# Optimization experiments

Measured on AMD Instinct MI355X. Metric: run time of the kernel, lower is better.

The kernel has to match this reference:

```python
import jax, jax.numpy as jnp
import numpy as np

N = 8  # node_count, complete graph
# edge list exactly as in __init__: all (i, j) with i != j, row-major order
_edges = np.array([[i, j] for i in range(N) for j in range(N) if i != j], dtype=np.int32)
SRC = jnp.asarray(_edges[:, 0])  # edge_index[0]
DST = jnp.asarray(_edges[:, 1])  # edge_index[1]


def gcn_norm_adj(edge_w):
    """Dense normalized adjacency D^-1/2 (A + I) D^-1/2 with edge weights, as in PyG GCNConv."""
    A = jnp.zeros((N, N), edge_w.dtype).at[DST, SRC].set(edge_w) + jnp.eye(N, dtype=edge_w.dtype)
    deg = A.sum(axis=1)  # in-degree (weights into each target node, incl. self loop)
    dinv = jnp.where(deg > 0, deg ** -0.5, 0.0)
    return dinv[:, None] * A * dinv[None, :]


def setup_inputs() -> dict:
    key = jax.random.key(0)
    ks = jax.random.split(key, 4)
    B, F_, H, O = 8192, 512, 256, 128
    return {
        "latent_vec": jax.random.normal(ks[0], (B, F_), jnp.float32),
        "node_features": jax.random.normal(ks[1], (N, F_), jnp.float32) * 0.1,
        "edge_attr": jnp.ones((N * (N - 1), 1), jnp.float32),
        "W1": jax.random.normal(ks[2], (F_, H), jnp.float32) / np.sqrt(F_),
        "b1": jnp.zeros((H,), jnp.float32),
        "W2": jax.random.normal(ks[3], (H, O), jnp.float32) / np.sqrt(H),
        "b2": jnp.zeros((O,), jnp.float32),
    }


def reference(latent_vec, node_features, edge_attr, W1, b1, W2, b2):
    # update_graph_with_latent: per-sample softmax perturbation of shared node features
    w = jax.nn.softmax(latent_vec[:, :N], axis=1)[..., None]        # [B, N, 1]
    X = node_features[None, :, :] + 0.1 * w                          # [B, N, F]
    A_hat = gcn_norm_adj(edge_attr[:, 0])                            # [N, N], shared across batch
    # GCNConv1 + ReLU (dropout is identity in eval mode)
    h = jax.nn.relu(jnp.einsum('ij,bjh->bih', A_hat, X @ W1) + b1)   # [B, N, H]
    # GCNConv2
    o = jnp.einsum('ij,bjo->bio', A_hat, h @ W2) + b2                # [B, N, O]
    return o.mean(axis=1)                                            # [B, O]
```

## Files before the change

kernel.cpp:

```cpp
#include <hip/hip_runtime.h>

#define NNODE 8
#define FDIM 512
#define HDIM 256
#define ODIM 128
#define BATCH 8192
#define SPB 16
#define NBLK (BATCH / SPB)

#define OCH 16
#define QCH (ODIM / OCH)
#define NGR 64
#define CHK (HDIM / NGR)

#define OFF_TAU  0
#define OFF_AHAT (NNODE * HDIM)
#define OFF_TAB  (OFF_AHAT + 128)

__global__ __launch_bounds__(1024) void gnn_build(
    const float* __restrict__ nf, const float* __restrict__ W1,
    const float* __restrict__ ea, const float* __restrict__ b1,
    const float* __restrict__ W2, const float* __restrict__ b2,
    float* __restrict__ ws)
{
    const int tid = threadIdx.x;
    const int j = blockIdx.x >> 3;
    const int q = blockIdx.x & (QCH - 1);
    const int obase = q * OCH;

    __shared__ float v_s[FDIM];
    __shared__ float pp_s[4][HDIM];
    __shared__ float ss_s[4][HDIM];
    __shared__ float A_s[64], dinv_s[NNODE], m_s[NNODE];
    __shared__ float P_s[HDIM], k_s[HDIM], tau_s[HDIM];
    __shared__ int   hs_s[HDIM];
    __shared__ int   rp_s[4][HDIM];
    __shared__ float pe_s[HDIM], ke_s[HDIM], bp_s[HDIM], bk_s[HDIM];
    __shared__ float cta[NGR][OCH], ctb[NGR][OCH], eta[NGR][OCH], etb[NGR][OCH];

    if (tid < 64) {
        int i = tid >> 3, qn = tid & 7;
        float a = (i == qn) ? 1.f : 0.f;
        if (i != qn) a += ea[qn * 7 + i - (i > qn ? 1 : 0)];
        A_s[tid] = a;
    }
    __syncthreads();
    if (tid < NNODE) {
        float d = 0.f;
#pragma unroll
        for (int qq = 0; qq < NNODE; qq++) d += A_s[tid * 8 + qq];
        dinv_s[tid] = d > 0.f ? 1.0f / sqrtf(d) : 0.f;
    }
    __syncthreads();
    if (tid < 64) {
        int i = tid >> 3, qn = tid & 7;
        A_s[tid] = dinv_s[i] * A_s[tid] * dinv_s[qn];
    }
    __syncthreads();
    if (tid < NNODE) {
        float mm = 0.f;
#pragma unroll
        for (int i = 0; i < NNODE; i++) mm += A_s[i * 8 + tid];
        m_s[tid] = mm * 0.125f;
    }
    if (tid < FDIM) {
        float v = 0.f;
#pragma unroll
        for (int n = 0; n < NNODE; n++) v = fmaf(A_s[j * 8 + n], nf[n * FDIM + tid], v);
        v_s[tid] = v;
    }
    __syncthreads();

    {
        const int h = tid & 255;
        const int g = tid >> 8;
        const float* Wp = W1 + (g * 128) * HDIM + h;
        const float* vp = v_s + g * 128;
        float pp = 0.f, ss = 0.f;
#pragma unroll 16
        for (int ff = 0; ff < 128; ff++) {
            float w = Wp[ff * HDIM];
            pp = fmaf(vp[ff], w, pp);
            ss += w;
        }
        pp_s[g][h] = pp;
        ss_s[g][h] = ss;
    }
    __syncthreads();

    if (tid < HDIM) {
        float P = b1[tid] + ((pp_s[0][tid] + pp_s[1][tid]) + (pp_s[2][tid] + pp_s[3][tid]));
        float s1 = ((ss_s[0][tid] + ss_s[1][tid]) + (ss_s[2][tid] + ss_s[3][tid]));
        float kap = 0.1f * s1;
        float tau = (kap != 0.f) ? (-P / kap) : __builtin_inff();
        P_s[tid] = P;
        k_s[tid] = kap;
        tau_s[tid] = tau;
        float mj = m_s[j];
        bp_s[tid] = mj * ((kap < 0.f || (kap == 0.f && P > 0.f)) ? P : 0.f);
        bk_s[tid] = mj * ((kap < 0.f) ? kap : 0.f);
    }
    __syncthreads();

    {
        const int h = tid & 255, kq = tid >> 8;
        float th = tau_s[h];
        int r = 0;
        for (int k = kq * 64; k < kq * 64 + 64; k++) {
            float tk = tau_s[k];
            r += (tk < th) || (tk == th && k < h);
        }
        rp_s[kq][h] = r;
    }
    __syncthreads();
    if (tid < HDIM) {
        int r = rp_s[0][tid] + rp_s[1][tid] + rp_s[2][tid] + rp_s[3][tid];
        hs_s[r] = tid;
        if (q == 0) ws[OFF_TAU + j * HDIM + r] = tau_s[tid];
    }
    if (blockIdx.x == 0 && tid >= 256 && tid < 320)
        ws[OFF_AHAT + tid - 256] = A_s[tid - 256];
    __syncthreads();
    if (tid < HDIM) {
        int h2 = hs_s[tid];
        float kk = k_s[h2], pp = P_s[h2];
        float sgn = (kk > 0.f) ? 1.f : ((kk < 0.f) ? -1.f : 0.f);
        float mj = m_s[j];
        pe_s[tid] = mj * sgn * pp;
        ke_s[tid] = mj * sgn * kk;
    }
    __syncthreads();

    const int oc = tid & (OCH - 1);
    const int rr = tid >> 4;
    {
        float ba = 0.f, bb = 0.f, sa = 0.f, sb = 0.f;
#pragma unroll
        for (int k = 0; k < CHK; k++) {
            int h = rr * CHK + k;
            float wb = W2[h * ODIM + obase + oc];
            ba = fmaf(bp_s[h], wb, ba);
            bb = fmaf(bk_s[h], wb, bb);
            float we = W2[hs_s[h] * ODIM + obase + oc];
            sa = fmaf(pe_s[h], we, sa);
            sb = fmaf(ke_s[h], we, sb);
        }
        cta[rr][oc] = ba; ctb[rr][oc] = bb;
        eta[rr][oc] = sa; etb[rr][oc] = sb;
    }
    __syncthreads();

    float2* TAB = (float2*)(ws + OFF_TAB);

    if (tid < OCH) {
        const int o = tid;
        float accA = 0.f, accB = 0.f;
#pragma unroll
        for (int g = 0; g < NGR; g++) { accA += cta[g][o]; accB += ctb[g][o]; }
        if (j == 0) accA += b2[obase + o];
        TAB[(size_t)(j * 257) * ODIM + obase + o] = make_float2(accA, accB);
#pragma unroll
        for (int g = 0; g < NGR; g++) {
            float ta = eta[g][o], tb = etb[g][o];
            eta[g][o] = accA; etb[g][o] = accB;
            accA += ta; accB += tb;
        }
    }
    __syncthreads();

    {
        float ra = eta[rr][oc], rb = etb[rr][oc];
#pragma unroll
        for (int k = 0; k < CHK; k++) {
            int r = rr * CHK + k;
            float we = W2[hs_s[r] * ODIM + obase + oc];
            ra = fmaf(pe_s[r], we, ra);
            rb = fmaf(ke_s[r], we, rb);
            TAB[(size_t)(j * 257 + r + 1) * ODIM + obase + oc] = make_float2(ra, rb);
        }
    }
}

__global__ __launch_bounds__(256) void gnn_main(const float* __restrict__ latent,
                                                const float* __restrict__ ws,
                                                float* __restrict__ out) {
    const int t = threadIdx.x;
    const int bs = blockIdx.x * SPB;

    __shared__ float tau_s[NNODE][HDIM];
    __shared__ float A_s[64];
    __shared__ float lat_s[SPB][NNODE];
    __shared__ float cc_s[SPB][NNODE];
    __shared__ int   rr_s[SPB][NNODE];

    for (int k = t; k < NNODE * HDIM; k += 256)
        ((float*)tau_s)[k] = ws[OFF_TAU + k];
    if (t < 64) A_s[t] = ws[OFF_AHAT + t];
    if (t >= 128) {
        int u = t - 128;
        int s = u >> 3, qq = u & 7;
        lat_s[s][qq] = latent[(size_t)(bs + s) * FDIM + qq];
    }
    __syncthreads();

    if (t < SPB * NNODE) {
        int s = t >> 3, i = t & 7;
        float mx = -1e30f;
#pragma unroll
        for (int qq = 0; qq < NNODE; qq++) mx = fmaxf(mx, lat_s[s][qq]);
        float sum = 0.f, acc = 0.f;
#pragma unroll
        for (int qq = 0; qq < NNODE; qq++) {
            float e = expf(lat_s[s][qq] - mx);
            sum += e;
            acc = fmaf(A_s[i * NNODE + qq], e, acc);
        }
        float c = acc / sum;
        cc_s[s][i] = c;
        int lo = 0, hi = HDIM;
        while (lo < hi) {
            int mid = (lo + hi) >> 1;
            if (tau_s[i][mid] < c) lo = mid + 1; else hi = mid;
        }
        rr_s[s][i] = lo;
    }
    __syncthreads();

    const int o = t & (ODIM - 1);
    const int sh = t >> 7;
    const float2* TAB = (const float2*)(ws + OFF_TAB);

#pragma unroll 2
    for (int s = sh; s < SPB; s += 2) {
        float acc = 0.f;
#pragma unroll
        for (int jj = 0; jj < NNODE; jj++) {
            int r = rr_s[s][jj];
            float c = cc_s[s][jj];
            float2 ab = TAB[(size_t)(jj * 257 + r) * ODIM + o];
            acc += fmaf(c, ab.y, ab.x);
        }
        out[(size_t)(bs + s) * ODIM + o] = acc;
    }
}

extern "C" void kernel_launch(void* const* d_in, const int* in_sizes, int n_in,
                              void* d_out, int out_size, void* d_ws, size_t ws_size,
                              hipStream_t stream) {
    const float* latent = (const float*)d_in[0];
    const float* nf     = (const float*)d_in[1];
    const float* ea     = (const float*)d_in[2];
    const float* W1     = (const float*)d_in[3];
    const float* b1     = (const float*)d_in[4];
    const float* W2     = (const float*)d_in[5];
    const float* b2     = (const float*)d_in[6];
    float* out = (float*)d_out;
    float* ws  = (float*)d_ws;

    hipLaunchKernelGGL(gnn_build, dim3(NNODE * QCH), dim3(1024), 0, stream,
                       nf, W1, ea, b1, W2, b2, ws);
    hipLaunchKernelGGL(gnn_main, dim3(NBLK), dim3(256), 0, stream, latent, ws, out);
}
```

Before: 25.73 us.

## Fuse build and main kernels into one launch with an atomic flag barrier

Merges the table-building kernel and the per-sample lookup kernel into a single 256-thread launch. The first 64 blocks build the tables and bump a global counter, and every block spins on that counter before reading the tables. Softmax and latent loading overlap with the build phase. The build work moves from 1024-thread to 256-thread blocks, so each thread does more serial work in the W1 reduction and the rank sort. It also adds a memset and relies on all build blocks being resident alongside the spinning ones, which risks a deadlock or long stalls.

```diff
diff --git a/kernel.cpp b/kernel.cpp
--- a/kernel.cpp
+++ b/kernel.cpp
@@ -10,33 +10,42 @@
 
 #define OCH 16
 #define QCH (ODIM / OCH)
-#define NGR 64
+#define NGR 16
 #define CHK (HDIM / NGR)
+#define NBUILD (NNODE * QCH)
 
 #define OFF_TAU  0
-#define OFF_AHAT (NNODE * HDIM)
-#define OFF_TAB  (OFF_AHAT + 128)
-
-__global__ __launch_bounds__(1024) void gnn_build(
-    const float* __restrict__ nf, const float* __restrict__ W1,
+#define OFF_TAB  (NNODE * HDIM)
+#define OFF_FLAG (OFF_TAB + NNODE * 257 * ODIM * 2)
+
+__global__ __launch_bounds__(256, 2) void gnn_one(
+    const float* __restrict__ latent, const float* __restrict__ nf,
     const float* __restrict__ ea, const float* __restrict__ b1,
-    const float* __restrict__ W2, const float* __restrict__ b2,
-    float* __restrict__ ws)
+    const float* __restrict__ W1, const float* __restrict__ W2,
+    const float* __restrict__ b2, float* __restrict__ ws,
+    float* __restrict__ out)
 {
     const int tid = threadIdx.x;
-    const int j = blockIdx.x >> 3;
-    const int q = blockIdx.x & (QCH - 1);
-    const int obase = q * OCH;
-
+    const int b = blockIdx.x;
+    const int bs = b * SPB;
+
+    __shared__ float A_s[64], dinv_s[NNODE], m_s[NNODE];
+    __shared__ float lat_s[SPB][NNODE];
+    __shared__ float cc_s[SPB][NNODE];
+    __shared__ int   rr_s[SPB][NNODE];
+    __shared__ float tau_m[NNODE][HDIM];
     __shared__ float v_s[FDIM];
-    __shared__ float pp_s[4][HDIM];
-    __shared__ float ss_s[4][HDIM];
-    __shared__ float A_s[64], dinv_s[NNODE], m_s[NNODE];
-    __shared__ float P_s[HDIM], k_s[HDIM], tau_s[HDIM];
+    __shared__ float P_s[HDIM], k_s[HDIM], tau_b[HDIM];
     __shared__ int   hs_s[HDIM];
-    __shared__ int   rp_s[4][HDIM];
     __shared__ float pe_s[HDIM], ke_s[HDIM], bp_s[HDIM], bk_s[HDIM];
     __shared__ float cta[NGR][OCH], ctb[NGR][OCH], eta[NGR][OCH], etb[NGR][OCH];
+
+    unsigned int* flag = (unsigned int*)(ws + OFF_FLAG);
+
+    if (tid >= 128) {
+        int u = tid - 128;
+        lat_s[u >> 3][u & 7] = latent[(size_t)(bs + (u >> 3)) * FDIM + (u & 7)];
+    }
 
     if (tid < 64) {
         int i = tid >> 3, qn = tid & 7;
@@ -63,148 +72,10 @@
         for (int i = 0; i < NNODE; i++) mm += A_s[i * 8 + tid];
         m_s[tid] = mm * 0.125f;
     }
-    if (tid < FDIM) {
-        float v = 0.f;
-#pragma unroll
-        for (int n = 0; n < NNODE; n++) v = fmaf(A_s[j * 8 + n], nf[n * FDIM + tid], v);
-        v_s[tid] = v;
-    }
-    __syncthreads();
-
-    {
-        const int h = tid & 255;
-        const int g = tid >> 8;
-        const float* Wp = W1 + (g * 128) * HDIM + h;
-        const float* vp = v_s + g * 128;
-        float pp = 0.f, ss = 0.f;
-#pragma unroll 16
-        for (int ff = 0; ff < 128; ff++) {
-            float w = Wp[ff * HDIM];
-            pp = fmaf(vp[ff], w, pp);
-            ss += w;
-        }
-        pp_s[g][h] = pp;
-        ss_s[g][h] = ss;
-    }
-    __syncthreads();
-
-    if (tid < HDIM) {
-        float P = b1[tid] + ((pp_s[0][tid] + pp_s[1][tid]) + (pp_s[2][tid] + pp_s[3][tid]));
-        float s1 = ((ss_s[0][tid] + ss_s[1][tid]) + (ss_s[2][tid] + ss_s[3][tid]));
-        float kap = 0.1f * s1;
-        float tau = (kap != 0.f) ? (-P / kap) : __builtin_inff();
-        P_s[tid] = P;
-        k_s[tid] = kap;
-        tau_s[tid] = tau;
-        float mj = m_s[j];
-        bp_s[tid] = mj * ((kap < 0.f || (kap == 0.f && P > 0.f)) ? P : 0.f);
-        bk_s[tid] = mj * ((kap < 0.f) ? kap : 0.f);
-    }
-    __syncthreads();
-
-    {
-        const int h = tid & 255, kq = tid >> 8;
-        float th = tau_s[h];
-        int r = 0;
-        for (int k = kq * 64; k < kq * 64 + 64; k++) {
-            float tk = tau_s[k];
-            r += (tk < th) || (tk == th && k < h);
-        }
-        rp_s[kq][h] = r;
-    }
-    __syncthreads();
-    if (tid < HDIM) {
-        int r = rp_s[0][tid] + rp_s[1][tid] + rp_s[2][tid] + rp_s[3][tid];
-        hs_s[r] = tid;
-        if (q == 0) ws[OFF_TAU + j * HDIM + r] = tau_s[tid];
-    }
-    if (blockIdx.x == 0 && tid >= 256 && tid < 320)
-        ws[OFF_AHAT + tid - 256] = A_s[tid - 256];
-    __syncthreads();
-    if (tid < HDIM) {
-        int h2 = hs_s[tid];
-        float kk = k_s[h2], pp = P_s[h2];
-        float sgn = (kk > 0.f) ? 1.f : ((kk < 0.f) ? -1.f : 0.f);
-        float mj = m_s[j];
-        pe_s[tid] = mj * sgn * pp;
-        ke_s[tid] = mj * sgn * kk;
-    }
-    __syncthreads();
-
-    const int oc = tid & (OCH - 1);
-    const int rr = tid >> 4;
-    {
-        float ba = 0.f, bb = 0.f, sa = 0.f, sb = 0.f;
-#pragma unroll
-        for (int k = 0; k < CHK; k++) {
-            int h = rr * CHK + k;
-            float wb = W2[h * ODIM + obase + oc];
-            ba = fmaf(bp_s[h], wb, ba);
-            bb = fmaf(bk_s[h], wb, bb);
-            float we = W2[hs_s[h] * ODIM + obase + oc];
-            sa = fmaf(pe_s[h], we, sa);
-            sb = fmaf(ke_s[h], we, sb);
-        }
-        cta[rr][oc] = ba; ctb[rr][oc] = bb;
-        eta[rr][oc] = sa; etb[rr][oc] = sb;
-    }
-    __syncthreads();
-
-    float2* TAB = (float2*)(ws + OFF_TAB);
-
-    if (tid < OCH) {
-        const int o = tid;
-        float accA = 0.f, accB = 0.f;
-#pragma unroll
-        for (int g = 0; g < NGR; g++) { accA += cta[g][o]; accB += ctb[g][o]; }
-        if (j == 0) accA += b2[obase + o];
-        TAB[(size_t)(j * 257) * ODIM + obase + o] = make_float2(accA, accB);
-#pragma unroll
-        for (int g = 0; g < NGR; g++) {
-            float ta = eta[g][o], tb = etb[g][o];
-            eta[g][o] = accA; etb[g][o] = accB;
-            accA += ta; accB += tb;
-        }
-    }
-    __syncthreads();
-
-    {
-        float ra = eta[rr][oc], rb = etb[rr][oc];
-#pragma unroll
-        for (int k = 0; k < CHK; k++) {
-            int r = rr * CHK + k;
-            float we = W2[hs_s[r] * ODIM + obase + oc];
-            ra = fmaf(pe_s[r], we, ra);
-            rb = fmaf(ke_s[r], we, rb);
-            TAB[(size_t)(j * 257 + r + 1) * ODIM + obase + oc] = make_float2(ra, rb);
-        }
-    }
-}
-
-__global__ __launch_bounds__(256) void gnn_main(const float* __restrict__ latent,
-                                                const float* __restrict__ ws,
-                                                float* __restrict__ out) {
-    const int t = threadIdx.x;
-    const int bs = blockIdx.x * SPB;
-
-    __shared__ float tau_s[NNODE][HDIM];
-    __shared__ float A_s[64];
-    __shared__ float lat_s[SPB][NNODE];
-    __shared__ float cc_s[SPB][NNODE];
-    __shared__ int   rr_s[SPB][NNODE];
-
-    for (int k = t; k < NNODE * HDIM; k += 256)
-        ((float*)tau_s)[k] = ws[OFF_TAU + k];
-    if (t < 64) A_s[t] = ws[OFF_AHAT + t];
-    if (t >= 128) {
-        int u = t - 128;
-        int s = u >> 3, qq = u & 7;
-        lat_s[s][qq] = latent[(size_t)(bs + s) * FDIM + qq];
-    }
-    __syncthreads();
-
-    if (t < SPB * NNODE) {
-        int s = t >> 3, i = t & 7;
+
+    float c_keep = 0.f;
+    if (tid < SPB * NNODE) {
+        int s = tid >> 3, i = tid & 7;
         float mx = -1e30f;
 #pragma unroll
         for (int qq = 0; qq < NNODE; qq++) mx = fmaxf(mx, lat_s[s][qq]);
@@ -215,19 +86,151 @@
             sum += e;
             acc = fmaf(A_s[i * NNODE + qq], e, acc);
         }
-        float c = acc / sum;
-        cc_s[s][i] = c;
+        c_keep = acc / sum;
+        cc_s[s][i] = c_keep;
+    }
+
+    if (b < NBUILD) {
+        const int j = b >> 3;
+        const int q = b & (QCH - 1);
+        const int obase = q * OCH;
+
+        {
+            float aj[NNODE];
+#pragma unroll
+            for (int n = 0; n < NNODE; n++) aj[n] = A_s[j * 8 + n];
+#pragma unroll
+            for (int u = 0; u < 2; u++) {
+                int f = tid + u * 256;
+                float v = 0.f;
+#pragma unroll
+                for (int n = 0; n < NNODE; n++) v = fmaf(aj[n], nf[n * FDIM + f], v);
+                v_s[f] = v;
+            }
+        }
+        __syncthreads();
+
+        {
+            const float* Wc = W1 + tid;
+            float pp = 0.f, ss = 0.f;
+#pragma unroll 8
+            for (int f = 0; f < FDIM; f++) {
+                float w = Wc[(size_t)f * HDIM];
+                pp = fmaf(v_s[f], w, pp);
+                ss += w;
+            }
+            float P = b1[tid] + pp;
+            float kap = 0.1f * ss;
+            float tau = (kap != 0.f) ? (-P / kap) : __builtin_inff();
+            P_s[tid] = P;
+            k_s[tid] = kap;
+            tau_b[tid] = tau;
+            float mj = m_s[j];
+            bp_s[tid] = mj * ((kap < 0.f || (kap == 0.f && P > 0.f)) ? P : 0.f);
+            bk_s[tid] = mj * ((kap < 0.f) ? kap : 0.f);
+        }
+        __syncthreads();
+
+        {
+            float th = tau_b[tid];
+            int r = 0;
+            for (int k = 0; k < HDIM; k++) {
+                float tk = tau_b[k];
+                r += (tk < th) || (tk == th && k < tid);
+            }
+            hs_s[r] = tid;
+            if (q == 0) ws[OFF_TAU + j * HDIM + r] = th;
+        }
+        __syncthreads();
+        {
+            int h2 = hs_s[tid];
+            float kk = k_s[h2], pp = P_s[h2];
+            float sgn = (kk > 0.f) ? 1.f : ((kk < 0.f) ? -1.f : 0.f);
+            float mj = m_s[j];
+            pe_s[tid] = mj * sgn * pp;
+            ke_s[tid] = mj * sgn * kk;
+        }
+        __syncthreads();
+
+        const int oc = tid & (OCH - 1);
+        const int rr = tid >> 4;
+        {
+            float ba = 0.f, bb = 0.f, sa = 0.f, sb = 0.f;
+#pragma unroll
+            for (int k = 0; k < CHK; k++) {
+                int h = rr * CHK + k;
+                float wb = W2[h * ODIM + obase + oc];
+                ba = fmaf(bp_s[h], wb, ba);
+                bb = fmaf(bk_s[h], wb, bb);
+                float we = W2[hs_s[h] * ODIM + obase + oc];
+                sa = fmaf(pe_s[h], we, sa);
+                sb = fmaf(ke_s[h], we, sb);
+            }
+            cta[rr][oc] = ba; ctb[rr][oc] = bb;
+            eta[rr][oc] = sa; etb[rr][oc] = sb;
+        }
+        __syncthreads();
+
+        float2* TAB = (float2*)(ws + OFF_TAB);
+
+        if (tid < OCH) {
+            const int o = tid;
+            float accA = 0.f, accB = 0.f;
+#pragma unroll
+            for (int g = 0; g < NGR; g++) { accA += cta[g][o]; accB += ctb[g][o]; }
+            if (j == 0) accA += b2[obase + o];
+            TAB[(size_t)(j * 257) * ODIM + obase + o] = make_float2(accA, accB);
+#pragma unroll
+            for (int g = 0; g < NGR; g++) {
+                float ta = eta[g][o], tb = etb[g][o];
+                eta[g][o] = accA; etb[g][o] = accB;
+                accA += ta; accB += tb;
+            }
+        }
+        __syncthreads();
+
+        {
+            float ra = eta[rr][oc], rb = etb[rr][oc];
+#pragma unroll
+            for (int k = 0; k < CHK; k++) {
+                int r = rr * CHK + k;
+                float we = W2[hs_s[r] * ODIM + obase + oc];
+                ra = fmaf(pe_s[r], we, ra);
+                rb = fmaf(ke_s[r], we, rb);
+                TAB[(size_t)(j * 257 + r + 1) * ODIM + obase + oc] = make_float2(ra, rb);
+            }
+        }
+        __syncthreads();
+        if (tid == 0)
+            __hip_atomic_fetch_add(flag, 1u, __ATOMIC_RELEASE, __HIP_MEMORY_SCOPE_AGENT);
+    }
+
+    if (tid == 0) {
+        while (__hip_atomic_fetch_add(flag, 0u, __ATOMIC_RELAXED,
+                                      __HIP_MEMORY_SCOPE_AGENT) < (unsigned)NBUILD)
+            __builtin_amdgcn_s_sleep(8);
+        __threadfence();
+    }
+    __syncthreads();
+
+    for (int k = tid; k < NNODE * HDIM; k += 256)
+        ((float*)tau_m)[k] = ws[OFF_TAU + k];
+    __syncthreads();
+
+    if (tid < SPB * NNODE) {
+        int s = tid >> 3, i = tid & 7;
+        float c = c_keep;
         int lo = 0, hi = HDIM;
         while (lo < hi) {
             int mid = (lo + hi) >> 1;
-            if (tau_s[i][mid] < c) lo = mid + 1; else hi = mid;
+            if (tau_m[i][mid] < c) lo = mid + 1; else hi = mid;
         }
         rr_s[s][i] = lo;
     }
     __syncthreads();
 
-    const int o = t & (ODIM - 1);
-    const int sh = t >> 7;
+    const int o = tid & (ODIM - 1);
+    const int sh = tid >> 7;
     const float2* TAB = (const float2*)(ws + OFF_TAB);
 
 #pragma unroll 2
@@ -257,7 +260,7 @@
     float* out = (float*)d_out;
     float* ws  = (float*)d_ws;
 
-    hipLaunchKernelGGL(gnn_build, dim3(NNODE * QCH), dim3(1024), 0, stream,
-                       nf, W1, ea, b1, W2, b2, ws);
-    hipLaunchKernelGGL(gnn_main, dim3(NBLK), dim3(256), 0, stream, latent, ws, out);
+    hipMemsetAsync((char*)d_ws + (size_t)OFF_FLAG * sizeof(float), 0, 4, stream);
+    hipLaunchKernelGGL(gnn_one, dim3(NBLK), dim3(256), 0, stream,
+                       latent, nf, ea, b1, W1, W2, b2, ws, out);
 }
```

Result: slower. 51.22 us (+99.1%).
